# Kernel optimization log

Hardware: AMD Instinct MI355X
Metric: run time of the kernel (lower is better)

Reference implementation:

```python
import jax, jax.numpy as jnp
import numpy as np

B, L, D, H = 48, 512, 192, 6
DK = D // H
HID = 4 * D
EPS = 1e-5
SCALE = 1.0 / np.float32(np.sqrt(DK))


def _ln(x, g, b):
    mu = x.mean(-1, keepdims=True)
    v = ((x - mu) ** 2).mean(-1, keepdims=True)
    return (x - mu) * jax.lax.rsqrt(v + EPS) * g + b


def _mln(x, m, g, b):
    # masked layernorm: valid rows normalized, invalid rows pass through unchanged
    return jnp.where(m[..., None], _ln(x, g, b), x)


def _mha(q, k, v, mask, wq, bq, wk, bk, wv, bv, wo, bo):
    def proj(x, w, bb):
        return (x @ w + bb).reshape(B, L, H, DK).transpose(0, 2, 1, 3)  # [B,H,L,dk]
    Q, K, V = proj(q, wq, bq), proj(k, wk, bk), proj(v, wv, bv)
    s = jnp.einsum('bhqd,bhkd->bhqk', Q, K) * SCALE
    s = jnp.where(mask[:, None], -1e9, s)  # mask True = invalid pair
    p = jax.nn.softmax(s, axis=-1)
    o = jnp.einsum('bhqk,bhkd->bhqd', p, V).transpose(0, 2, 1, 3).reshape(B, L, D)
    return o @ wo + bo


def _forward(x_a, x_b, valid_a, valid_b,
             ln_a_g, ln_a_b, ln_b_g, ln_b_b, ln_oa_g, ln_oa_b, ln_ob_g, ln_ob_b,
             wq, bq, wk, bk, wv, bv, wo, bo,
             fln_g, fln_b, flno_g, flno_b, w1, b1, w2, b2):
    mB2A = ~(valid_a[:, :, None] & valid_b[:, None, :])  # [B,La,Lb]
    mA2B = ~(valid_b[:, :, None] & valid_a[:, None, :])
    a = _mln(x_a, valid_a, ln_a_g, ln_a_b)
    b = _mln(x_b, valid_b, ln_b_g, ln_b_b)
    oa = _mha(a, b, b, mB2A, wq, bq, wk, bk, wv, bv, wo, bo)
    oa = _mln(oa + x_a, valid_a, ln_oa_g, ln_oa_b)
    ob = _mha(b, a, a, mA2B, wq, bq, wk, bk, wv, bv, wo, bo)
    ob = _mln(ob + x_b, valid_b, ln_ob_g, ln_ob_b)

    def ffn(x, m):
        xn = _mln(x, m, fln_g, fln_b)
        y = jax.nn.gelu(xn @ w1 + b1, approximate=False) @ w2 + b2
        return _mln(x + y, m, flno_g, flno_b)

    return ffn(oa, valid_a), ffn(ob, valid_b)


def setup_inputs() -> dict:
    key = jax.random.key(0)
    ks = jax.random.split(key, 12)
    p = lambda k, s: jax.random.normal(k, s, dtype=jnp.float32) * 0.02
    ones = lambda s: jnp.ones(s, dtype=jnp.float32)
    zeros = lambda s: jnp.zeros(s, dtype=jnp.float32)
    return {
        'x_a': jax.random.normal(ks[0], (B, L, D), dtype=jnp.float32),
        'x_b': jax.random.normal(ks[1], (B, L, D), dtype=jnp.float32),
        'valid_a': jax.random.bernoulli(ks[2], 0.9, (B, L)),
        'valid_b': jax.random.bernoulli(ks[3], 0.9, (B, L)),
        'ln_a_g': ones((D,)), 'ln_a_b': zeros((D,)),
        'ln_b_g': ones((D,)), 'ln_b_b': zeros((D,)),
        'ln_oa_g': ones((D,)), 'ln_oa_b': zeros((D,)),
        'ln_ob_g': ones((D,)), 'ln_ob_b': zeros((D,)),
        'wq': p(ks[4], (D, D)), 'bq': zeros((D,)),
        'wk': p(ks[5], (D, D)), 'bk': zeros((D,)),
        'wv': p(ks[6], (D, D)), 'bv': zeros((D,)),
        'wo': p(ks[7], (D, D)), 'bo': zeros((D,)),
        'fln_g': ones((D,)), 'fln_b': zeros((D,)),
        'flno_g': ones((D,)), 'flno_b': zeros((D,)),
        'w1': p(ks[8], (D, HID)), 'b1': zeros((HID,)),
        'w2': p(ks[9], (HID, D)), 'b2': zeros((D,)),
    }


def reference(x_a, x_b, valid_a, valid_b,
              ln_a_g, ln_a_b, ln_b_g, ln_b_b, ln_oa_g, ln_oa_b, ln_ob_g, ln_ob_b,
              wq, bq, wk, bk, wv, bv, wo, bo,
              fln_g, fln_b, flno_g, flno_b, w1, b1, w2, b2):
    return _forward(x_a, x_b, valid_a, valid_b,
                    ln_a_g, ln_a_b, ln_b_g, ln_b_b, ln_oa_g, ln_oa_b, ln_ob_g, ln_ob_b,
                    wq, bq, wk, bk, wv, bv, wo, bo,
                    fln_g, fln_b, flno_g, flno_b, w1, b1, w2, b2)
```

## Files before the change

kernel.cpp:

```cpp
#include <hip/hip_runtime.h>
#include <math.h>

#define BB 48
#define LL 512
#define DD 192
#define HH 6
#define DKK 32
#define HID 768
#define ROWS (BB * LL)
#define BLD ((size_t)ROWS * DD)
#define SB2 0.25503531f
#define MASKED_X (-36.0f)

typedef unsigned short ushort_t;
typedef unsigned int uint_t;
typedef __bf16 bf16x8 __attribute__((ext_vector_type(8)));
typedef float f32x4 __attribute__((ext_vector_type(4)));

union U4BF8 { uint4 u; bf16x8 b; };
union BFU { __bf16 h; ushort_t u; };

__device__ __forceinline__ ushort_t f2bf(float f) {
  union { float f; uint_t u; } v; v.f = f;
  uint_t r = v.u + 0x7fffu + ((v.u >> 16) & 1u);
  return (ushort_t)(r >> 16);
}
__device__ __forceinline__ ushort_t cvt_bf(float f) {
  BFU c; c.h = (__bf16)f; return c.u;
}

__device__ __forceinline__ int swz_w(int n, int k, int N) {
  return ((k >> 5) * (N >> 4) + (n >> 4)) * 512 +
         ((((k & 31) >> 3) << 4) + (n & 15)) * 8 + (k & 7);
}

__global__ __launch_bounds__(256) void pack_kernel(
    const float* __restrict__ wq, const float* __restrict__ wk,
    const float* __restrict__ wv, const float* __restrict__ wo,
    const float* __restrict__ w1, const float* __restrict__ w2,
    const float* __restrict__ bq, const float* __restrict__ bk,
    const float* __restrict__ bv,
    ushort_t* __restrict__ Wqkv, ushort_t* __restrict__ Wo,
    ushort_t* __restrict__ W1, ushort_t* __restrict__ W2,
    float* __restrict__ bqkv) {
  int i = blockIdx.x * 256 + threadIdx.x;
  if (i < 110592) {
    int n2 = i / 192, k = i - n2 * 192;
    int part = n2 / 192, n = n2 - part * 192;
    const float* src = part == 0 ? wq : (part == 1 ? wk : wv);
    Wqkv[swz_w(n2, k, 576)] = f2bf(src[k * 192 + n]);
  } else if (i < 147456) {
    int j = i - 110592;
    int n = j / 192, k = j - n * 192;
    Wo[swz_w(n, k, 192)] = f2bf(wo[k * 192 + n]);
  } else if (i < 294912) {
    int j = i - 147456;
    int n = j / 192, k = j - n * 192;
    W1[j] = f2bf(w1[k * 768 + n]);
  } else if (i < 442368) {
    int j = i - 294912;
    int n = j / 768, k = j - n * 768;
    W2[j] = f2bf(w2[k * 192 + n]);
  } else if (i < 442944) {
    int j = i - 442368;
    bqkv[j] = j < 192 ? bq[j] : (j < 384 ? bk[j - 192] : bv[j - 384]);
  }
}

__global__ __launch_bounds__(256) void qkv_ln_kernel(
    const float* __restrict__ xa, const float* __restrict__ xb,
    const int* __restrict__ va, const int* __restrict__ vb,
    const float* __restrict__ g_a, const float* __restrict__ b_a,
    const float* __restrict__ g_b, const float* __restrict__ b_b,
    const ushort_t* __restrict__ Wsw, const float* __restrict__ bias,
    ushort_t* __restrict__ Cb) {
  constexpr int N = 576;
  constexpr int CSB = N + 8;
  __shared__ ushort_t smem[32 * CSB];
  ushort_t* As = smem;

  int tid = threadIdx.x;
  int w = tid >> 6, lane = tid & 63, l15 = lane & 15, kq = lane >> 4;
  int row0 = blockIdx.x * 32;
  int side = row0 >= ROWS;
  int rb = row0 - side * ROWS;

  {
    int row = tid >> 3, l8 = tid & 7;
    const float* xr = (side ? xb : xa) + (size_t)(rb + row) * DD + l8 * 24;
    float v[24];
    float s = 0.f;
#pragma unroll
    for (int j = 0; j < 6; ++j) {
      float4 q = *(const float4*)(xr + j * 4);
      v[j*4+0] = q.x; v[j*4+1] = q.y; v[j*4+2] = q.z; v[j*4+3] = q.w;
      s += q.x + q.y + q.z + q.w;
    }
    s += __shfl_xor(s, 1); s += __shfl_xor(s, 2); s += __shfl_xor(s, 4);
    float mu = s * (1.0f / 192.0f);
    float ss = 0.f;
#pragma unroll
    for (int j = 0; j < 24; ++j) { float d = v[j] - mu; ss += d * d; }
    ss += __shfl_xor(ss, 1); ss += __shfl_xor(ss, 2); ss += __shfl_xor(ss, 4);
    float inv = rsqrtf(ss * (1.0f / 192.0f) + 1e-5f);
    int vld = (side ? vb : va)[rb + row];
    const float* g = side ? g_b : g_a;
    const float* be = side ? b_b : b_a;
    ushort_t ob[24];
#pragma unroll
    for (int j = 0; j < 24; ++j) {
      int col = l8 * 24 + j;
      float r = vld ? (v[j] - mu) * inv * g[col] + be[col] : v[j];
      ob[j] = f2bf(r);
    }
#pragma unroll
    for (int j = 0; j < 3; ++j)
      *(uint4*)(&As[row * 200 + l8 * 24 + j * 8]) = *(const uint4*)(&ob[j * 8]);
  }
  __syncthreads();

  f32x4 acc[2][9];
#pragma unroll
  for (int qs = 0; qs < 2; ++qs)
#pragma unroll
    for (int nt = 0; nt < 9; ++nt) acc[qs][nt] = (f32x4){0.f, 0.f, 0.f, 0.f};

#pragma unroll 1
  for (int kk = 0; kk < 6; ++kk) {
    bf16x8 af[2];
#pragma unroll
    for (int qs = 0; qs < 2; ++qs)
      af[qs] = *(const bf16x8*)(&As[(qs * 16 + l15) * 200 + kk * 32 + kq * 8]);
    const ushort_t* wp =
        Wsw + ((size_t)(kk * (N >> 4) + w * 9) << 9) + lane * 8;
#pragma unroll
    for (int nt = 0; nt < 9; ++nt) {
      U4BF8 wf;
      wf.u = *(const uint4*)(wp + (nt << 9));
#pragma unroll
      for (int qs = 0; qs < 2; ++qs)
        acc[qs][nt] = __builtin_amdgcn_mfma_f32_16x16x32_bf16(
            af[qs], wf.b, acc[qs][nt], 0, 0, 0);
    }
  }
  __syncthreads();

  ushort_t* Cs = smem;
#pragma unroll
  for (int nt = 0; nt < 9; ++nt) {
    int col = (w * 9 + nt) * 16 + l15;
    float bb = bias[col];
#pragma unroll
    for (int qs = 0; qs < 2; ++qs)
#pragma unroll
      for (int r = 0; r < 4; ++r)
        Cs[(qs * 16 + kq * 4 + r) * CSB + col] = f2bf(acc[qs][nt][r] + bb);
  }
  __syncthreads();
  constexpr int UPR = (N * 2) / 16;
#pragma unroll
  for (int i = 0; i < (32 * UPR) / 256; ++i) {
    int idx = tid + i * 256;
    int r = idx / UPR, u = idx - r * UPR;
    *(uint4*)(Cb + (size_t)row0 * N + idx * 8) =
        *(const uint4*)(&Cs[r * CSB + u * 8]);
  }
}

__global__ __launch_bounds__(256) void oproj_ln_kernel(
    const ushort_t* __restrict__ A, const ushort_t* __restrict__ Wsw,
    const float* __restrict__ bias,
    const float* __restrict__ xa, const float* __restrict__ xb,
    const int* __restrict__ va, const int* __restrict__ vb,
    const float* __restrict__ g_oa, const float* __restrict__ b_oa,
    const float* __restrict__ g_ob, const float* __restrict__ b_ob,
    const float* __restrict__ g_f, const float* __restrict__ b_f,
    float* __restrict__ outf, ushort_t* __restrict__ outb) {
  __shared__ float smemf[32 * 196];
  ushort_t* As = (ushort_t*)smemf;

  int tid = threadIdx.x;
  int w = tid >> 6, lane = tid & 63, l15 = lane & 15, kq = lane >> 4;
  int row0 = blockIdx.x * 32;
  int side = row0 >= ROWS;
  int rb = row0 - side * ROWS;

  {
    const ushort_t* ap = A + (size_t)row0 * DD;
#pragma unroll
    for (int i = 0; i < 3; ++i) {
      int idx = tid + i * 256;
      int r = idx / 24, c = (idx - r * 24) * 8;
      *(uint4*)(&As[r * 200 + c]) = *(const uint4*)(ap + idx * 8);
    }
  }
  __syncthreads();

  f32x4 acc[2][3];
#pragma unroll
  for (int qs = 0; qs < 2; ++qs)
#pragma unroll
    for (int nt = 0; nt < 3; ++nt) acc[qs][nt] = (f32x4){0.f, 0.f, 0.f, 0.f};

#pragma unroll 1
  for (int kk = 0; kk < 6; ++kk) {
    bf16x8 af[2];
#pragma unroll
    for (int qs = 0; qs < 2; ++qs)
      af[qs] = *(const bf16x8*)(&As[(qs * 16 + l15) * 200 + kk * 32 + kq * 8]);
    const ushort_t* wp =
        Wsw + ((size_t)(kk * (192 >> 4) + w * 3) << 9) + lane * 8;
#pragma unroll
    for (int nt = 0; nt < 3; ++nt) {
      U4BF8 wf;
      wf.u = *(const uint4*)(wp + (nt << 9));
#pragma unroll
      for (int qs = 0; qs < 2; ++qs)
        acc[qs][nt] = __builtin_amdgcn_mfma_f32_16x16x32_bf16(
            af[qs], wf.b, acc[qs][nt], 0, 0, 0);
    }
  }
  __syncthreads();

  float* Cs = smemf;
#pragma unroll
  for (int nt = 0; nt < 3; ++nt) {
    int col = (w * 3 + nt) * 16 + l15;
    float bb = bias[col];
#pragma unroll
    for (int qs = 0; qs < 2; ++qs)
#pragma unroll
      for (int r = 0; r < 4; ++r)
        Cs[(qs * 16 + kq * 4 + r) * 196 + col] = acc[qs][nt][r] + bb;
  }
  __syncthreads();

  int row = tid >> 3, l8 = tid & 7;
  int grow = row0 + row;
  const float* xrow = (side ? xb : xa) + (size_t)(rb + row) * DD;
  const float* crow = &Cs[row * 196];
  float v[24];
  float s = 0.f;
#pragma unroll
  for (int j = 0; j < 6; ++j) {
    int col = j * 32 + l8 * 4;
    float4 q = *(const float4*)(xrow + col);
    v[j*4+0] = crow[col+0] + q.x; v[j*4+1] = crow[col+1] + q.y;
    v[j*4+2] = crow[col+2] + q.z; v[j*4+3] = crow[col+3] + q.w;
    s += v[j*4+0] + v[j*4+1] + v[j*4+2] + v[j*4+3];
  }
  s += __shfl_xor(s, 1); s += __shfl_xor(s, 2); s += __shfl_xor(s, 4);
  float mu = s * (1.0f / 192.0f);
  float ss = 0.f;
#pragma unroll
  for (int j = 0; j < 24; ++j) { float d = v[j] - mu; ss += d * d; }
  ss += __shfl_xor(ss, 1); ss += __shfl_xor(ss, 2); ss += __shfl_xor(ss, 4);
  float inv = rsqrtf(ss * (1.0f / 192.0f) + 1e-5f);
  int vld = (side ? vb : va)[rb + row];
  const float* g1 = side ? g_ob : g_oa;
  const float* b1 = side ? b_ob : b_oa;
  float y[24];
#pragma unroll
  for (int j = 0; j < 6; ++j) {
#pragma unroll
    for (int e = 0; e < 4; ++e) {
      int col = j * 32 + l8 * 4 + e;
      float vv = v[j * 4 + e];
      y[j * 4 + e] = vld ? (vv - mu) * inv * g1[col] + b1[col] : vv;
    }
  }
  float* orow = outf + (size_t)grow * DD;
#pragma unroll
  for (int j = 0; j < 6; ++j) {
    float4 q = {y[j*4+0], y[j*4+1], y[j*4+2], y[j*4+3]};
    *(float4*)(orow + j * 32 + l8 * 4) = q;
  }
  float s2 = 0.f;
#pragma unroll
  for (int j = 0; j < 24; ++j) s2 += y[j];
  s2 += __shfl_xor(s2, 1); s2 += __shfl_xor(s2, 2); s2 += __shfl_xor(s2, 4);
  float mu2 = s2 * (1.0f / 192.0f);
  float ss2 = 0.f;
#pragma unroll
  for (int j = 0; j < 24; ++j) { float e = y[j] - mu2; ss2 += e * e; }
  ss2 += __shfl_xor(ss2, 1); ss2 += __shfl_xor(ss2, 2); ss2 += __shfl_xor(ss2, 4);
  float inv2 = rsqrtf(ss2 * (1.0f / 192.0f) + 1e-5f);
  ushort_t* obrow = outb + (size_t)grow * DD;
#pragma unroll
  for (int j = 0; j < 6; ++j) {
    ushort_t zb[4];
#pragma unroll
    for (int e = 0; e < 4; ++e) {
      int col = j * 32 + l8 * 4 + e;
      float z = vld ? (y[j*4+e] - mu2) * inv2 * g_f[col] + b_f[col] : y[j*4+e];
      zb[e] = f2bf(z);
    }
    *(uint2*)(obrow + j * 32 + l8 * 4) = *(const uint2*)(&zb[0]);
  }
}

__global__ __launch_bounds__(256, 3) void ffn_fused_kernel(
    const ushort_t* __restrict__ A, const ushort_t* __restrict__ W1t,
    const float* __restrict__ bias1, const ushort_t* __restrict__ W2t,
    const float* __restrict__ bias2,
    const int* __restrict__ va, const int* __restrict__ vb,
    const float* __restrict__ g_f, const float* __restrict__ b_f,
    float* __restrict__ outf) {
  __shared__ float smemf[64 * 196];
  ushort_t* As = (ushort_t*)smemf;
  ushort_t* Hs = As + 64 * 200;

  int tid = threadIdx.x;
  int w = tid >> 6;
  int lane = tid & 63;
  int l15 = lane & 15;
  int kq = lane >> 4;
  int row0 = blockIdx.x * 64;
  int side = row0 >= ROWS;
  int rb0 = row0 - side * ROWS;

#pragma unroll
  for (int i = 0; i < 6; ++i) {
    int idx = tid + i * 256;
    int r = idx / 24, c = (idx % 24) * 8;
    *(uint4*)(&As[r * 200 + c]) = *(const uint4*)(A + (size_t)(row0 + r) * DD + c);
  }

  const ushort_t* w1p = W1t + (size_t)(w * 16 + l15) * DD + kq * 8;
  const ushort_t* w2p = W2t + (size_t)(w * 48 + l15) * HID + kq * 8;

  U4BF8 w1f[6], w1n[6], w2f[6];
#pragma unroll
  for (int kk = 0; kk < 6; ++kk)
    w1f[kk].u = *(const uint4*)(w1p + kk * 32);

  f32x4 Cacc[4][3];
#pragma unroll
  for (int qs = 0; qs < 4; ++qs)
#pragma unroll
    for (int nt = 0; nt < 3; ++nt) Cacc[qs][nt] = (f32x4){0.f, 0.f, 0.f, 0.f};

  __syncthreads();

  for (int hc = 0; hc < 12; ++hc) {
#pragma unroll
    for (int kk2 = 0; kk2 < 2; ++kk2)
#pragma unroll
      for (int nt = 0; nt < 3; ++nt)
        w2f[kk2 * 3 + nt].u =
            *(const uint4*)(w2p + (size_t)(nt * 16) * HID + hc * 64 + kk2 * 32);

    f32x4 Hacc[4];
#pragma unroll
    for (int qs = 0; qs < 4; ++qs) Hacc[qs] = (f32x4){0.f, 0.f, 0.f, 0.f};
#pragma unroll
    for (int kk = 0; kk < 6; ++kk) {
#pragma unroll
      for (int qs = 0; qs < 4; ++qs) {
        bf16x8 af = *(const bf16x8*)(&As[(qs * 16 + l15) * 200 + kk * 32 + kq * 8]);
        Hacc[qs] = __builtin_amdgcn_mfma_f32_16x16x32_bf16(
            af, w1f[kk].b, Hacc[qs], 0, 0, 0);
      }
    }

    if (hc < 11) {
#pragma unroll
      for (int kk = 0; kk < 6; ++kk)
        w1n[kk].u = *(const uint4*)(w1p + (size_t)(hc + 1) * 64 * DD + kk * 32);
    }

    {
      float bb = bias1[hc * 64 + w * 16 + l15];
      ushort_t* hb = &Hs[(hc & 1) * 4608];
#pragma unroll
      for (int qs = 0; qs < 4; ++qs)
#pragma unroll
        for (int r = 0; r < 4; ++r) {
          float x = Hacc[qs][r] + bb;
          x = 0.5f * x * (1.0f + erff(x * 0.70710678118654752f));
          hb[(qs * 16 + kq * 4 + r) * 72 + w * 16 + l15] = f2bf(x);
        }
    }
    __syncthreads();

#pragma unroll
    for (int kk2 = 0; kk2 < 2; ++kk2) {
      bf16x8 hf[4];
#pragma unroll
      for (int qs = 0; qs < 4; ++qs)
        hf[qs] = *(const bf16x8*)(&Hs[(hc & 1) * 4608 +
                                      (qs * 16 + l15) * 72 + kk2 * 32 + kq * 8]);
#pragma unroll
      for (int nt = 0; nt < 3; ++nt)
#pragma unroll
        for (int qs = 0; qs < 4; ++qs)
          Cacc[qs][nt] = __builtin_amdgcn_mfma_f32_16x16x32_bf16(
              hf[qs], w2f[kk2 * 3 + nt].b, Cacc[qs][nt], 0, 0, 0);
    }

#pragma unroll
    for (int kk = 0; kk < 6; ++kk) w1f[kk] = w1n[kk];
  }
  __syncthreads();

  float* Cs = smemf;
#pragma unroll
  for (int qs = 0; qs < 4; ++qs)
#pragma unroll
    for (int nt = 0; nt < 3; ++nt) {
      int col = w * 48 + nt * 16 + l15;
      float bb = bias2[col];
#pragma unroll
      for (int r = 0; r < 4; ++r)
        Cs[(qs * 16 + kq * 4 + r) * 196 + col] = Cacc[qs][nt][r] + bb;
    }
  __syncthreads();

  int row = tid >> 2, l4 = tid & 3;
  int grow = row0 + row;
  float* orow = outf + (size_t)grow * DD;
  const float* crow = &Cs[row * 196];
  float v[48];
  float s = 0.f;
#pragma unroll
  for (int j = 0; j < 12; ++j) {
    int col = j * 16 + l4 * 4;
    float4 q = *(const float4*)(orow + col);
    v[j*4+0] = crow[col+0] + q.x; v[j*4+1] = crow[col+1] + q.y;
    v[j*4+2] = crow[col+2] + q.z; v[j*4+3] = crow[col+3] + q.w;
    s += v[j*4+0] + v[j*4+1] + v[j*4+2] + v[j*4+3];
  }
  s += __shfl_xor(s, 1); s += __shfl_xor(s, 2);
  float mu = s * (1.0f / 192.0f);
  float ss = 0.f;
#pragma unroll
  for (int j = 0; j < 48; ++j) { float d = v[j] - mu; ss += d * d; }
  ss += __shfl_xor(ss, 1); ss += __shfl_xor(ss, 2);
  float inv = rsqrtf(ss * (1.0f / 192.0f) + 1e-5f);
  int vld = (side ? vb : va)[rb0 + row];
#pragma unroll
  for (int j = 0; j < 12; ++j) {
    int col = j * 16 + l4 * 4;
    float4 q;
#pragma unroll
    for (int e = 0; e < 4; ++e) {
      float vv = v[j * 4 + e];
      ((float*)&q)[e] = vld ? (vv - mu) * inv * g_f[col + e] + b_f[col + e] : vv;
    }
    *(float4*)(orow + col) = q;
  }
}

__global__ __launch_bounds__(256) void attn_mfma_kernel(
    const ushort_t* __restrict__ QKV,
    const int* __restrict__ valid_a, const int* __restrict__ valid_b,
    ushort_t* __restrict__ out) {
  int i = blockIdx.x;
  int gid = ((i >> 5) << 3) | (i & 7);
  int qt = (i >> 3) & 3;
  int side = gid >= BB * HH;
  int grem = side ? gid - BB * HH : gid;
  int h = grem % HH;
  int batch = grem / HH;
  int tid = threadIdx.x;
  int w = tid >> 6;
  int lane = tid & 63;
  int l15 = lane & 15;
  int kq = lane >> 4;

  const int* validq = side ? valid_b : valid_a;
  const int* validk = side ? valid_a : valid_b;
  size_t qrow0  = (size_t)side * ROWS + (size_t)batch * LL;
  size_t kvrow0 = (size_t)(1 - side) * ROWS + (size_t)batch * LL;

  __shared__ ushort_t VsT[2][32 * 72];
  __shared__ ushort_t Ps[4][32 * 72];

  int qbase = qt * 128 + w * 32;

  U4BF8 qfrag[2];
#pragma unroll
  for (int qs = 0; qs < 2; ++qs)
    qfrag[qs].u = *(const uint4*)(QKV + (qrow0 + qbase + qs * 16 + l15) * 576 +
                                  h * DKK + kq * 8);

  float sqf[2][4], mq[2][4];
#pragma unroll
  for (int qs = 0; qs < 2; ++qs)
#pragma unroll
    for (int r = 0; r < 4; ++r) {
      int vq = validq[batch * LL + qbase + qs * 16 + kq * 4 + r];
      sqf[qs][r] = vq ? SB2 : 0.0f;
      mq[qs][r]  = vq ? 0.0f : MASKED_X;
    }

  float lsum[2][4];
  f32x4 Oacc[2][2];
#pragma unroll
  for (int qs = 0; qs < 2; ++qs) {
#pragma unroll
    for (int r = 0; r < 4; ++r) lsum[qs][r] = 0.0f;
#pragma unroll
    for (int ds = 0; ds < 2; ++ds) Oacc[qs][ds] = (f32x4){0.f, 0.f, 0.f, 0.f};
  }

  uint4 vv = *(const uint4*)(QKV + (kvrow0 + lane) * 576 + 384 + h * DKK + w * 8);
  U4BF8 kf[4];
  int vki[4];
#pragma unroll
  for (int ks = 0; ks < 4; ++ks) {
    kf[ks].u = *(const uint4*)(QKV + (kvrow0 + ks * 16 + l15) * 576 +
                               192 + h * DKK + kq * 8);
    vki[ks] = validk[batch * LL + ks * 16 + l15];
  }

  for (int c = 0; c < LL; c += 64) {
    int buf = (c >> 6) & 1;
    {
      uint_t uu[4] = {vv.x, vv.y, vv.z, vv.w};
#pragma unroll
      for (int j = 0; j < 4; ++j) {
        VsT[buf][(w * 8 + 2 * j) * 72 + lane]     = (ushort_t)(uu[j] & 0xffffu);
        VsT[buf][(w * 8 + 2 * j + 1) * 72 + lane] = (ushort_t)(uu[j] >> 16);
      }
    }
    uint4 vvn;
    if (c + 64 < LL)
      vvn = *(const uint4*)(QKV + (kvrow0 + c + 64 + lane) * 576 +
                            384 + h * DKK + w * 8);
    __syncthreads();

    f32x4 S[2][4];
    __builtin_amdgcn_s_setprio(1);
#pragma unroll
    for (int ks = 0; ks < 4; ++ks)
#pragma unroll
      for (int qs = 0; qs < 2; ++qs) {
        f32x4 z = (f32x4){0.f, 0.f, 0.f, 0.f};
        S[qs][ks] = __builtin_amdgcn_mfma_f32_16x16x32_bf16(
            qfrag[qs].b, kf[ks].b, z, 0, 0, 0);
      }
    __builtin_amdgcn_s_setprio(0);

    float mkb[4];
#pragma unroll
    for (int ks = 0; ks < 4; ++ks) mkb[ks] = vki[ks] ? 0.0f : MASKED_X;

    U4BF8 kfn[4];
    int vkn[4];
    if (c + 64 < LL) {
#pragma unroll
      for (int ks = 0; ks < 4; ++ks) {
        kfn[ks].u = *(const uint4*)(QKV + (kvrow0 + c + 64 + ks * 16 + l15) * 576 +
                                    192 + h * DKK + kq * 8);
        vkn[ks] = validk[batch * LL + c + 64 + ks * 16 + l15];
      }
    }

#pragma unroll
    for (int qs = 0; qs < 2; ++qs)
#pragma unroll
      for (int ks = 0; ks < 4; ++ks)
#pragma unroll
        for (int r = 0; r < 4; ++r) {
          float xs = fmaf(S[qs][ks][r], sqf[qs][r], fminf(mq[qs][r], mkb[ks]));
          float p = __builtin_amdgcn_exp2f(xs);
          lsum[qs][r] += p;
          Ps[w][(qs * 16 + kq * 4 + r) * 72 + ks * 16 + l15] = cvt_bf(p);
        }

    __builtin_amdgcn_s_setprio(1);
#pragma unroll
    for (int kh = 0; kh < 2; ++kh) {
      bf16x8 pf[2], vf[2];
#pragma unroll
      for (int qs = 0; qs < 2; ++qs)
        pf[qs] = *(const bf16x8*)(&Ps[w][(qs * 16 + l15) * 72 + kh * 32 + kq * 8]);
#pragma unroll
      for (int ds = 0; ds < 2; ++ds)
        vf[ds] = *(const bf16x8*)(&VsT[buf][(ds * 16 + l15) * 72 + kh * 32 + kq * 8]);
#pragma unroll
      for (int qs = 0; qs < 2; ++qs)
#pragma unroll
        for (int ds = 0; ds < 2; ++ds)
          Oacc[qs][ds] = __builtin_amdgcn_mfma_f32_16x16x32_bf16(
              pf[qs], vf[ds], Oacc[qs][ds], 0, 0, 0);
    }
    __builtin_amdgcn_s_setprio(0);

    vv = vvn;
#pragma unroll
    for (int ks = 0; ks < 4; ++ks) { kf[ks] = kfn[ks]; vki[ks] = vkn[ks]; }
  }

#pragma unroll
  for (int qs = 0; qs < 2; ++qs)
#pragma unroll
    for (int r = 0; r < 4; ++r) {
      float sm = lsum[qs][r];
#pragma unroll
      for (int off = 1; off < 16; off <<= 1) sm += __shfl_xor(sm, off);
      lsum[qs][r] = sm;
    }

#pragma unroll
  for (int qs = 0; qs < 2; ++qs)
#pragma unroll
    for (int ds = 0; ds < 2; ++ds)
#pragma unroll
      for (int r = 0; r < 4; ++r) {
        int q = qbase + qs * 16 + kq * 4 + r;
        out[(qrow0 + q) * DD + h * DKK + ds * 16 + l15] =
            f2bf(Oacc[qs][ds][r] / lsum[qs][r]);
      }
}

extern "C" void kernel_launch(void* const* d_in, const int* in_sizes, int n_in,
                              void* d_out, int out_size, void* d_ws, size_t ws_size,
                              hipStream_t stream) {
  const float* x_a = (const float*)d_in[0];
  const float* x_b = (const float*)d_in[1];
  const int* valid_a = (const int*)d_in[2];
  const int* valid_b = (const int*)d_in[3];
  const float* ln_a_g = (const float*)d_in[4];
  const float* ln_a_b = (const float*)d_in[5];
  const float* ln_b_g = (const float*)d_in[6];
  const float* ln_b_b = (const float*)d_in[7];
  const float* ln_oa_g = (const float*)d_in[8];
  const float* ln_oa_b = (const float*)d_in[9];
  const float* ln_ob_g = (const float*)d_in[10];
  const float* ln_ob_b = (const float*)d_in[11];
  const float* wq = (const float*)d_in[12];
  const float* bq = (const float*)d_in[13];
  const float* wk = (const float*)d_in[14];
  const float* bk = (const float*)d_in[15];
  const float* wv = (const float*)d_in[16];
  const float* bv = (const float*)d_in[17];
  const float* wo = (const float*)d_in[18];
  const float* bo = (const float*)d_in[19];
  const float* fln_g = (const float*)d_in[20];
  const float* fln_b = (const float*)d_in[21];
  const float* flno_g = (const float*)d_in[22];
  const float* flno_b = (const float*)d_in[23];
  const float* w1 = (const float*)d_in[24];
  const float* b1 = (const float*)d_in[25];
  const float* w2 = (const float*)d_in[26];
  const float* b2 = (const float*)d_in[27];

  char* wsb = (char*)d_ws;
  ushort_t* Wqkv = (ushort_t*)wsb;
  ushort_t* Wo_t = Wqkv + 110592;
  ushort_t* W1_t = Wo_t + 36864;
  ushort_t* W2_t = W1_t + 147456;
  float*    bqkv = (float*)(W2_t + 147456);
  ushort_t* lnFull = (ushort_t*)(wsb + 887040);
  ushort_t* attO   = lnFull;
  ushort_t* QKV = (ushort_t*)(wsb + 19761408);

  float* out_a = (float*)d_out;

  dim3 b256(256);
  dim3 gGemm(2 * ROWS / 32);
  dim3 gAttn(BB * HH * 4 * 2);
  dim3 gFFN(2 * ROWS / 64);

  hipLaunchKernelGGL(pack_kernel, dim3(1731), b256, 0, stream,
                     wq, wk, wv, wo, w1, w2, bq, bk, bv,
                     Wqkv, Wo_t, W1_t, W2_t, bqkv);

  hipLaunchKernelGGL(qkv_ln_kernel, gGemm, b256, 0, stream,
                     x_a, x_b, valid_a, valid_b,
                     ln_a_g, ln_a_b, ln_b_g, ln_b_b,
                     Wqkv, bqkv, QKV);

  hipLaunchKernelGGL(attn_mfma_kernel, gAttn, b256, 0, stream,
                     QKV, valid_a, valid_b, attO);

  hipLaunchKernelGGL(oproj_ln_kernel, gGemm, b256, 0, stream,
                     attO, Wo_t, bo, x_a, x_b, valid_a, valid_b,
                     ln_oa_g, ln_oa_b, ln_ob_g, ln_ob_b, fln_g, fln_b,
                     out_a, lnFull);

  hipLaunchKernelGGL(ffn_fused_kernel, gFFN, b256, 0, stream,
                     lnFull, W1_t, b1, W2_t, b2, valid_a, valid_b,
                     flno_g, flno_b, out_a);
}
```

Baseline: 357.5 us.

## Shrink FFN tile to 32 rows with two waves covering wider columns

Restructures the fused FFN kernel to process 32 rows per block with 128 threads, where each wave computes 32 hidden columns and 96 output columns instead of 16 and 48. It removes the register double-buffered prefetch of W1 fragments and loads them inline per k-step, which lowers register pressure and doubles grid size for more parallelism. The trade-off is twice as many total weight fetches per row from L2, and W1 load latency is no longer hidden by prefetch.

```diff
diff --git a/kernel.cpp b/kernel.cpp
--- a/kernel.cpp
+++ b/kernel.cpp
@@ -299,116 +299,115 @@
   }
 }
 
-__global__ __launch_bounds__(256, 3) void ffn_fused_kernel(
+__global__ __launch_bounds__(128, 3) void ffn_fused_kernel(
     const ushort_t* __restrict__ A, const ushort_t* __restrict__ W1t,
     const float* __restrict__ bias1, const ushort_t* __restrict__ W2t,
     const float* __restrict__ bias2,
     const int* __restrict__ va, const int* __restrict__ vb,
     const float* __restrict__ g_f, const float* __restrict__ b_f,
     float* __restrict__ outf) {
-  __shared__ float smemf[64 * 196];
+  __shared__ float smemf[32 * 196];
   ushort_t* As = (ushort_t*)smemf;
-  ushort_t* Hs = As + 64 * 200;
+  ushort_t* Hs = As + 32 * 200;
 
   int tid = threadIdx.x;
   int w = tid >> 6;
   int lane = tid & 63;
   int l15 = lane & 15;
   int kq = lane >> 4;
-  int row0 = blockIdx.x * 64;
+  int row0 = blockIdx.x * 32;
   int side = row0 >= ROWS;
   int rb0 = row0 - side * ROWS;
 
 #pragma unroll
   for (int i = 0; i < 6; ++i) {
-    int idx = tid + i * 256;
+    int idx = tid + i * 128;
     int r = idx / 24, c = (idx % 24) * 8;
     *(uint4*)(&As[r * 200 + c]) = *(const uint4*)(A + (size_t)(row0 + r) * DD + c);
   }
 
-  const ushort_t* w1p = W1t + (size_t)(w * 16 + l15) * DD + kq * 8;
-  const ushort_t* w2p = W2t + (size_t)(w * 48 + l15) * HID + kq * 8;
-
-  U4BF8 w1f[6], w1n[6], w2f[6];
-#pragma unroll
-  for (int kk = 0; kk < 6; ++kk)
-    w1f[kk].u = *(const uint4*)(w1p + kk * 32);
-
-  f32x4 Cacc[4][3];
-#pragma unroll
-  for (int qs = 0; qs < 4; ++qs)
-#pragma unroll
-    for (int nt = 0; nt < 3; ++nt) Cacc[qs][nt] = (f32x4){0.f, 0.f, 0.f, 0.f};
+  const ushort_t* w1p = W1t + (size_t)(w * 32 + l15) * DD + kq * 8;
+  const ushort_t* w2p = W2t + (size_t)(w * 96 + l15) * HID + kq * 8;
+
+  f32x4 Cacc[2][6];
+#pragma unroll
+  for (int qs = 0; qs < 2; ++qs)
+#pragma unroll
+    for (int nt = 0; nt < 6; ++nt) Cacc[qs][nt] = (f32x4){0.f, 0.f, 0.f, 0.f};
 
   __syncthreads();
 
   for (int hc = 0; hc < 12; ++hc) {
+    U4BF8 w2f[12];
 #pragma unroll
     for (int kk2 = 0; kk2 < 2; ++kk2)
 #pragma unroll
-      for (int nt = 0; nt < 3; ++nt)
-        w2f[kk2 * 3 + nt].u =
+      for (int nt = 0; nt < 6; ++nt)
+        w2f[kk2 * 6 + nt].u =
             *(const uint4*)(w2p + (size_t)(nt * 16) * HID + hc * 64 + kk2 * 32);
 
-    f32x4 Hacc[4];
-#pragma unroll
-    for (int qs = 0; qs < 4; ++qs) Hacc[qs] = (f32x4){0.f, 0.f, 0.f, 0.f};
+    f32x4 Hacc[2][2];
+#pragma unroll
+    for (int qs = 0; qs < 2; ++qs)
+#pragma unroll
+      for (int nt = 0; nt < 2; ++nt) Hacc[qs][nt] = (f32x4){0.f, 0.f, 0.f, 0.f};
 #pragma unroll
     for (int kk = 0; kk < 6; ++kk) {
-#pragma unroll
-      for (int qs = 0; qs < 4; ++qs) {
-        bf16x8 af = *(const bf16x8*)(&As[(qs * 16 + l15) * 200 + kk * 32 + kq * 8]);
-        Hacc[qs] = __builtin_amdgcn_mfma_f32_16x16x32_bf16(
-            af, w1f[kk].b, Hacc[qs], 0, 0, 0);
+      bf16x8 af[2];
+#pragma unroll
+      for (int qs = 0; qs < 2; ++qs)
+        af[qs] = *(const bf16x8*)(&As[(qs * 16 + l15) * 200 + kk * 32 + kq * 8]);
+#pragma unroll
+      for (int nt = 0; nt < 2; ++nt) {
+        U4BF8 wf;
+        wf.u = *(const uint4*)(w1p + (size_t)(hc * 64 + nt * 16) * DD + kk * 32);
+#pragma unroll
+        for (int qs = 0; qs < 2; ++qs)
+          Hacc[qs][nt] = __builtin_amdgcn_mfma_f32_16x16x32_bf16(
+              af[qs], wf.b, Hacc[qs][nt], 0, 0, 0);
       }
     }
 
-    if (hc < 11) {
-#pragma unroll
-      for (int kk = 0; kk < 6; ++kk)
-        w1n[kk].u = *(const uint4*)(w1p + (size_t)(hc + 1) * 64 * DD + kk * 32);
-    }
-
     {
-      float bb = bias1[hc * 64 + w * 16 + l15];
-      ushort_t* hb = &Hs[(hc & 1) * 4608];
-#pragma unroll
-      for (int qs = 0; qs < 4; ++qs)
-#pragma unroll
-        for (int r = 0; r < 4; ++r) {
-          float x = Hacc[qs][r] + bb;
-          x = 0.5f * x * (1.0f + erff(x * 0.70710678118654752f));
-          hb[(qs * 16 + kq * 4 + r) * 72 + w * 16 + l15] = f2bf(x);
-        }
+      ushort_t* hb = &Hs[(hc & 1) * 2304];
+#pragma unroll
+      for (int nt = 0; nt < 2; ++nt) {
+        float bb = bias1[hc * 64 + w * 32 + nt * 16 + l15];
+#pragma unroll
+        for (int qs = 0; qs < 2; ++qs)
+#pragma unroll
+          for (int r = 0; r < 4; ++r) {
+            float x = Hacc[qs][nt][r] + bb;
+            x = 0.5f * x * (1.0f + erff(x * 0.70710678118654752f));
+            hb[(qs * 16 + kq * 4 + r) * 72 + w * 32 + nt * 16 + l15] = f2bf(x);
+          }
+      }
     }
     __syncthreads();
 
 #pragma unroll
     for (int kk2 = 0; kk2 < 2; ++kk2) {
-      bf16x8 hf[4];
-#pragma unroll
-      for (int qs = 0; qs < 4; ++qs)
-        hf[qs] = *(const bf16x8*)(&Hs[(hc & 1) * 4608 +
+      bf16x8 hf[2];
+#pragma unroll
+      for (int qs = 0; qs < 2; ++qs)
+        hf[qs] = *(const bf16x8*)(&Hs[(hc & 1) * 2304 +
                                       (qs * 16 + l15) * 72 + kk2 * 32 + kq * 8]);
 #pragma unroll
-      for (int nt = 0; nt < 3; ++nt)
-#pragma unroll
-        for (int qs = 0; qs < 4; ++qs)
+      for (int nt = 0; nt < 6; ++nt)
+#pragma unroll
+        for (int qs = 0; qs < 2; ++qs)
           Cacc[qs][nt] = __builtin_amdgcn_mfma_f32_16x16x32_bf16(
-              hf[qs], w2f[kk2 * 3 + nt].b, Cacc[qs][nt], 0, 0, 0);
-    }
-
-#pragma unroll
-    for (int kk = 0; kk < 6; ++kk) w1f[kk] = w1n[kk];
+              hf[qs], w2f[kk2 * 6 + nt].b, Cacc[qs][nt], 0, 0, 0);
+    }
   }
   __syncthreads();
 
   float* Cs = smemf;
 #pragma unroll
-  for (int qs = 0; qs < 4; ++qs)
-#pragma unroll
-    for (int nt = 0; nt < 3; ++nt) {
-      int col = w * 48 + nt * 16 + l15;
+  for (int qs = 0; qs < 2; ++qs)
+#pragma unroll
+    for (int nt = 0; nt < 6; ++nt) {
+      int col = w * 96 + nt * 16 + l15;
       float bb = bias2[col];
 #pragma unroll
       for (int r = 0; r < 4; ++r)
@@ -659,10 +658,10 @@
 
   float* out_a = (float*)d_out;
 
-  dim3 b256(256);
+  dim3 b128(128), b256(256);
   dim3 gGemm(2 * ROWS / 32);
   dim3 gAttn(BB * HH * 4 * 2);
-  dim3 gFFN(2 * ROWS / 64);
+  dim3 gFFN(2 * ROWS / 32);
 
   hipLaunchKernelGGL(pack_kernel, dim3(1731), b256, 0, stream,
                      wq, wk, wv, wo, w1, w2, bq, bk, bv,
@@ -681,7 +680,7 @@
                      ln_oa_g, ln_oa_b, ln_ob_g, ln_ob_b, fln_g, fln_b,
                      out_a, lnFull);
 
-  hipLaunchKernelGGL(ffn_fused_kernel, gFFN, b256, 0, stream,
+  hipLaunchKernelGGL(ffn_fused_kernel, gFFN, b128, 0, stream,
                      lnFull, W1_t, b1, W2_t, b2, valid_a, valid_b,
                      flno_g, flno_b, out_a);
 }
```

Result: slower. 404.6 us (+13.2%).

## Fuse output projection and layernorms into FFN kernel, keep residual in registers

Applied to the files above, without the earlier changes.

Merges the O-projection and double-layernorm kernel into the fused FFN kernel, so each 64-row block computes the Wo GEMM, both layernorms, and then the FFN without writing the fp32 residual and the bf16 normalized activations to global memory and reading them back. The residual is held in registers (y[48]) across the FFN, and the normalized bf16 rows are written directly into shared memory as the FFN input. This removes one launch and a round trip of intermediates through global memory. In exchange it raises register pressure under a launch bound of 3 blocks per SM, which may cause spills or lower occupancy, and the O-projection now runs with 64-row tiles instead of 32.

```diff
diff --git a/kernel.cpp b/kernel.cpp
--- a/kernel.cpp
+++ b/kernel.cpp
@@ -167,154 +167,25 @@
   }
 }
 
-__global__ __launch_bounds__(256) void oproj_ln_kernel(
-    const ushort_t* __restrict__ A, const ushort_t* __restrict__ Wsw,
-    const float* __restrict__ bias,
+__global__ __launch_bounds__(256, 3) void oproj_ffn_kernel(
+    const ushort_t* __restrict__ A, const ushort_t* __restrict__ Wosw,
+    const float* __restrict__ bo,
     const float* __restrict__ xa, const float* __restrict__ xb,
     const int* __restrict__ va, const int* __restrict__ vb,
     const float* __restrict__ g_oa, const float* __restrict__ b_oa,
     const float* __restrict__ g_ob, const float* __restrict__ b_ob,
     const float* __restrict__ g_f, const float* __restrict__ b_f,
-    float* __restrict__ outf, ushort_t* __restrict__ outb) {
-  __shared__ float smemf[32 * 196];
-  ushort_t* As = (ushort_t*)smemf;
-
-  int tid = threadIdx.x;
-  int w = tid >> 6, lane = tid & 63, l15 = lane & 15, kq = lane >> 4;
-  int row0 = blockIdx.x * 32;
-  int side = row0 >= ROWS;
-  int rb = row0 - side * ROWS;
-
-  {
-    const ushort_t* ap = A + (size_t)row0 * DD;
-#pragma unroll
-    for (int i = 0; i < 3; ++i) {
-      int idx = tid + i * 256;
-      int r = idx / 24, c = (idx - r * 24) * 8;
-      *(uint4*)(&As[r * 200 + c]) = *(const uint4*)(ap + idx * 8);
-    }
-  }
-  __syncthreads();
-
-  f32x4 acc[2][3];
-#pragma unroll
-  for (int qs = 0; qs < 2; ++qs)
-#pragma unroll
-    for (int nt = 0; nt < 3; ++nt) acc[qs][nt] = (f32x4){0.f, 0.f, 0.f, 0.f};
-
-#pragma unroll 1
-  for (int kk = 0; kk < 6; ++kk) {
-    bf16x8 af[2];
-#pragma unroll
-    for (int qs = 0; qs < 2; ++qs)
-      af[qs] = *(const bf16x8*)(&As[(qs * 16 + l15) * 200 + kk * 32 + kq * 8]);
-    const ushort_t* wp =
-        Wsw + ((size_t)(kk * (192 >> 4) + w * 3) << 9) + lane * 8;
-#pragma unroll
-    for (int nt = 0; nt < 3; ++nt) {
-      U4BF8 wf;
-      wf.u = *(const uint4*)(wp + (nt << 9));
-#pragma unroll
-      for (int qs = 0; qs < 2; ++qs)
-        acc[qs][nt] = __builtin_amdgcn_mfma_f32_16x16x32_bf16(
-            af[qs], wf.b, acc[qs][nt], 0, 0, 0);
-    }
-  }
-  __syncthreads();
-
-  float* Cs = smemf;
-#pragma unroll
-  for (int nt = 0; nt < 3; ++nt) {
-    int col = (w * 3 + nt) * 16 + l15;
-    float bb = bias[col];
-#pragma unroll
-    for (int qs = 0; qs < 2; ++qs)
-#pragma unroll
-      for (int r = 0; r < 4; ++r)
-        Cs[(qs * 16 + kq * 4 + r) * 196 + col] = acc[qs][nt][r] + bb;
-  }
-  __syncthreads();
-
-  int row = tid >> 3, l8 = tid & 7;
-  int grow = row0 + row;
-  const float* xrow = (side ? xb : xa) + (size_t)(rb + row) * DD;
-  const float* crow = &Cs[row * 196];
-  float v[24];
-  float s = 0.f;
-#pragma unroll
-  for (int j = 0; j < 6; ++j) {
-    int col = j * 32 + l8 * 4;
-    float4 q = *(const float4*)(xrow + col);
-    v[j*4+0] = crow[col+0] + q.x; v[j*4+1] = crow[col+1] + q.y;
-    v[j*4+2] = crow[col+2] + q.z; v[j*4+3] = crow[col+3] + q.w;
-    s += v[j*4+0] + v[j*4+1] + v[j*4+2] + v[j*4+3];
-  }
-  s += __shfl_xor(s, 1); s += __shfl_xor(s, 2); s += __shfl_xor(s, 4);
-  float mu = s * (1.0f / 192.0f);
-  float ss = 0.f;
-#pragma unroll
-  for (int j = 0; j < 24; ++j) { float d = v[j] - mu; ss += d * d; }
-  ss += __shfl_xor(ss, 1); ss += __shfl_xor(ss, 2); ss += __shfl_xor(ss, 4);
-  float inv = rsqrtf(ss * (1.0f / 192.0f) + 1e-5f);
-  int vld = (side ? vb : va)[rb + row];
-  const float* g1 = side ? g_ob : g_oa;
-  const float* b1 = side ? b_ob : b_oa;
-  float y[24];
-#pragma unroll
-  for (int j = 0; j < 6; ++j) {
-#pragma unroll
-    for (int e = 0; e < 4; ++e) {
-      int col = j * 32 + l8 * 4 + e;
-      float vv = v[j * 4 + e];
-      y[j * 4 + e] = vld ? (vv - mu) * inv * g1[col] + b1[col] : vv;
-    }
-  }
-  float* orow = outf + (size_t)grow * DD;
-#pragma unroll
-  for (int j = 0; j < 6; ++j) {
-    float4 q = {y[j*4+0], y[j*4+1], y[j*4+2], y[j*4+3]};
-    *(float4*)(orow + j * 32 + l8 * 4) = q;
-  }
-  float s2 = 0.f;
-#pragma unroll
-  for (int j = 0; j < 24; ++j) s2 += y[j];
-  s2 += __shfl_xor(s2, 1); s2 += __shfl_xor(s2, 2); s2 += __shfl_xor(s2, 4);
-  float mu2 = s2 * (1.0f / 192.0f);
-  float ss2 = 0.f;
-#pragma unroll
-  for (int j = 0; j < 24; ++j) { float e = y[j] - mu2; ss2 += e * e; }
-  ss2 += __shfl_xor(ss2, 1); ss2 += __shfl_xor(ss2, 2); ss2 += __shfl_xor(ss2, 4);
-  float inv2 = rsqrtf(ss2 * (1.0f / 192.0f) + 1e-5f);
-  ushort_t* obrow = outb + (size_t)grow * DD;
-#pragma unroll
-  for (int j = 0; j < 6; ++j) {
-    ushort_t zb[4];
-#pragma unroll
-    for (int e = 0; e < 4; ++e) {
-      int col = j * 32 + l8 * 4 + e;
-      float z = vld ? (y[j*4+e] - mu2) * inv2 * g_f[col] + b_f[col] : y[j*4+e];
-      zb[e] = f2bf(z);
-    }
-    *(uint2*)(obrow + j * 32 + l8 * 4) = *(const uint2*)(&zb[0]);
-  }
-}
-
-__global__ __launch_bounds__(256, 3) void ffn_fused_kernel(
-    const ushort_t* __restrict__ A, const ushort_t* __restrict__ W1t,
-    const float* __restrict__ bias1, const ushort_t* __restrict__ W2t,
-    const float* __restrict__ bias2,
-    const int* __restrict__ va, const int* __restrict__ vb,
-    const float* __restrict__ g_f, const float* __restrict__ b_f,
+    const ushort_t* __restrict__ W1t, const float* __restrict__ bias1,
+    const ushort_t* __restrict__ W2t, const float* __restrict__ bias2,
+    const float* __restrict__ g_fo, const float* __restrict__ b_fo,
     float* __restrict__ outf) {
   __shared__ float smemf[64 * 196];
   ushort_t* As = (ushort_t*)smemf;
   ushort_t* Hs = As + 64 * 200;
+  float* Cs = smemf;
 
   int tid = threadIdx.x;
-  int w = tid >> 6;
-  int lane = tid & 63;
-  int l15 = lane & 15;
-  int kq = lane >> 4;
+  int w = tid >> 6, lane = tid & 63, l15 = lane & 15, kq = lane >> 4;
   int row0 = blockIdx.x * 64;
   int side = row0 >= ROWS;
   int rb0 = row0 - side * ROWS;
@@ -325,6 +196,99 @@
     int r = idx / 24, c = (idx % 24) * 8;
     *(uint4*)(&As[r * 200 + c]) = *(const uint4*)(A + (size_t)(row0 + r) * DD + c);
   }
+  __syncthreads();
+
+  f32x4 Cacc[4][3];
+#pragma unroll
+  for (int qs = 0; qs < 4; ++qs)
+#pragma unroll
+    for (int nt = 0; nt < 3; ++nt) Cacc[qs][nt] = (f32x4){0.f, 0.f, 0.f, 0.f};
+
+#pragma unroll 1
+  for (int kk = 0; kk < 6; ++kk) {
+    bf16x8 af[4];
+#pragma unroll
+    for (int qs = 0; qs < 4; ++qs)
+      af[qs] = *(const bf16x8*)(&As[(qs * 16 + l15) * 200 + kk * 32 + kq * 8]);
+    const ushort_t* wp = Wosw + ((size_t)(kk * 12 + w * 3) << 9) + lane * 8;
+#pragma unroll
+    for (int nt = 0; nt < 3; ++nt) {
+      U4BF8 wf;
+      wf.u = *(const uint4*)(wp + (nt << 9));
+#pragma unroll
+      for (int qs = 0; qs < 4; ++qs)
+        Cacc[qs][nt] = __builtin_amdgcn_mfma_f32_16x16x32_bf16(
+            af[qs], wf.b, Cacc[qs][nt], 0, 0, 0);
+    }
+  }
+  __syncthreads();
+
+#pragma unroll
+  for (int qs = 0; qs < 4; ++qs)
+#pragma unroll
+    for (int nt = 0; nt < 3; ++nt) {
+      int col = w * 48 + nt * 16 + l15;
+      float bb = bo[col];
+#pragma unroll
+      for (int r = 0; r < 4; ++r)
+        Cs[(qs * 16 + kq * 4 + r) * 196 + col] = Cacc[qs][nt][r] + bb;
+    }
+  __syncthreads();
+
+  int row = tid >> 2, l4 = tid & 3;
+  int vld = (side ? vb : va)[rb0 + row];
+  const float* xrow = (side ? xb : xa) + (size_t)(rb0 + row) * DD;
+  const float* crow = &Cs[row * 196];
+  const float* g1 = side ? g_ob : g_oa;
+  const float* b1 = side ? b_ob : b_oa;
+  float y[48];
+  float s = 0.f;
+#pragma unroll
+  for (int j = 0; j < 12; ++j) {
+    int col = j * 16 + l4 * 4;
+    float4 q = *(const float4*)(xrow + col);
+    y[j*4+0] = crow[col+0] + q.x; y[j*4+1] = crow[col+1] + q.y;
+    y[j*4+2] = crow[col+2] + q.z; y[j*4+3] = crow[col+3] + q.w;
+    s += y[j*4+0] + y[j*4+1] + y[j*4+2] + y[j*4+3];
+  }
+  s += __shfl_xor(s, 1); s += __shfl_xor(s, 2);
+  float mu = s * (1.0f / 192.0f);
+  float ss = 0.f;
+#pragma unroll
+  for (int j = 0; j < 48; ++j) { float d = y[j] - mu; ss += d * d; }
+  ss += __shfl_xor(ss, 1); ss += __shfl_xor(ss, 2);
+  float inv = rsqrtf(ss * (1.0f / 192.0f) + 1e-5f);
+#pragma unroll
+  for (int j = 0; j < 12; ++j)
+#pragma unroll
+    for (int e = 0; e < 4; ++e) {
+      int col = j * 16 + l4 * 4 + e;
+      float vv = y[j * 4 + e];
+      y[j * 4 + e] = vld ? (vv - mu) * inv * g1[col] + b1[col] : vv;
+    }
+  float s2 = 0.f;
+#pragma unroll
+  for (int j = 0; j < 48; ++j) s2 += y[j];
+  s2 += __shfl_xor(s2, 1); s2 += __shfl_xor(s2, 2);
+  float mu2 = s2 * (1.0f / 192.0f);
+  float ss2 = 0.f;
+#pragma unroll
+  for (int j = 0; j < 48; ++j) { float e = y[j] - mu2; ss2 += e * e; }
+  ss2 += __shfl_xor(ss2, 1); ss2 += __shfl_xor(ss2, 2);
+  float inv2 = rsqrtf(ss2 * (1.0f / 192.0f) + 1e-5f);
+  ushort_t z[48];
+#pragma unroll
+  for (int j = 0; j < 12; ++j)
+#pragma unroll
+    for (int e = 0; e < 4; ++e) {
+      int col = j * 16 + l4 * 4 + e;
+      float zz = vld ? (y[j*4+e] - mu2) * inv2 * g_f[col] + b_f[col] : y[j*4+e];
+      z[j * 4 + e] = f2bf(zz);
+    }
+  __syncthreads();
+#pragma unroll
+  for (int j = 0; j < 12; ++j)
+    *(uint2*)(&As[row * 200 + j * 16 + l4 * 4]) = *(const uint2*)(&z[j * 4]);
 
   const ushort_t* w1p = W1t + (size_t)(w * 16 + l15) * DD + kq * 8;
   const ushort_t* w2p = W2t + (size_t)(w * 48 + l15) * HID + kq * 8;
@@ -334,11 +298,11 @@
   for (int kk = 0; kk < 6; ++kk)
     w1f[kk].u = *(const uint4*)(w1p + kk * 32);
 
-  f32x4 Cacc[4][3];
+  f32x4 Facc[4][3];
 #pragma unroll
   for (int qs = 0; qs < 4; ++qs)
 #pragma unroll
-    for (int nt = 0; nt < 3; ++nt) Cacc[qs][nt] = (f32x4){0.f, 0.f, 0.f, 0.f};
+    for (int nt = 0; nt < 3; ++nt) Facc[qs][nt] = (f32x4){0.f, 0.f, 0.f, 0.f};
 
   __syncthreads();
 
@@ -394,8 +358,8 @@
       for (int nt = 0; nt < 3; ++nt)
 #pragma unroll
         for (int qs = 0; qs < 4; ++qs)
-          Cacc[qs][nt] = __builtin_amdgcn_mfma_f32_16x16x32_bf16(
-              hf[qs], w2f[kk2 * 3 + nt].b, Cacc[qs][nt], 0, 0, 0);
+          Facc[qs][nt] = __builtin_amdgcn_mfma_f32_16x16x32_bf16(
+              hf[qs], w2f[kk2 * 3 + nt].b, Facc[qs][nt], 0, 0, 0);
     }
 
 #pragma unroll
@@ -403,7 +367,6 @@
   }
   __syncthreads();
 
-  float* Cs = smemf;
 #pragma unroll
   for (int qs = 0; qs < 4; ++qs)
 #pragma unroll
@@ -412,40 +375,37 @@
       float bb = bias2[col];
 #pragma unroll
       for (int r = 0; r < 4; ++r)
-        Cs[(qs * 16 + kq * 4 + r) * 196 + col] = Cacc[qs][nt][r] + bb;
-    }
-  __syncthreads();
-
-  int row = tid >> 2, l4 = tid & 3;
-  int grow = row0 + row;
-  float* orow = outf + (size_t)grow * DD;
-  const float* crow = &Cs[row * 196];
-  float v[48];
-  float s = 0.f;
+        Cs[(qs * 16 + kq * 4 + r) * 196 + col] = Facc[qs][nt][r] + bb;
+    }
+  __syncthreads();
+
+  float* orow = outf + (size_t)(row0 + row) * DD;
+  float s3 = 0.f;
 #pragma unroll
   for (int j = 0; j < 12; ++j) {
     int col = j * 16 + l4 * 4;
-    float4 q = *(const float4*)(orow + col);
-    v[j*4+0] = crow[col+0] + q.x; v[j*4+1] = crow[col+1] + q.y;
-    v[j*4+2] = crow[col+2] + q.z; v[j*4+3] = crow[col+3] + q.w;
-    s += v[j*4+0] + v[j*4+1] + v[j*4+2] + v[j*4+3];
-  }
-  s += __shfl_xor(s, 1); s += __shfl_xor(s, 2);
-  float mu = s * (1.0f / 192.0f);
-  float ss = 0.f;
-#pragma unroll
-  for (int j = 0; j < 48; ++j) { float d = v[j] - mu; ss += d * d; }
-  ss += __shfl_xor(ss, 1); ss += __shfl_xor(ss, 2);
-  float inv = rsqrtf(ss * (1.0f / 192.0f) + 1e-5f);
-  int vld = (side ? vb : va)[rb0 + row];
+#pragma unroll
+    for (int e = 0; e < 4; ++e) {
+      y[j * 4 + e] += crow[col + e];
+      s3 += y[j * 4 + e];
+    }
+  }
+  s3 += __shfl_xor(s3, 1); s3 += __shfl_xor(s3, 2);
+  float mu3 = s3 * (1.0f / 192.0f);
+  float ss3 = 0.f;
+#pragma unroll
+  for (int j = 0; j < 48; ++j) { float d = y[j] - mu3; ss3 += d * d; }
+  ss3 += __shfl_xor(ss3, 1); ss3 += __shfl_xor(ss3, 2);
+  float inv3 = rsqrtf(ss3 * (1.0f / 192.0f) + 1e-5f);
 #pragma unroll
   for (int j = 0; j < 12; ++j) {
     int col = j * 16 + l4 * 4;
     float4 q;
 #pragma unroll
     for (int e = 0; e < 4; ++e) {
-      float vv = v[j * 4 + e];
-      ((float*)&q)[e] = vld ? (vv - mu) * inv * g_f[col + e] + b_f[col + e] : vv;
+      float vv = y[j * 4 + e];
+      ((float*)&q)[e] =
+          vld ? (vv - mu3) * inv3 * g_fo[col + e] + b_fo[col + e] : vv;
     }
     *(float4*)(orow + col) = q;
   }
@@ -653,8 +613,7 @@
   ushort_t* W1_t = Wo_t + 36864;
   ushort_t* W2_t = W1_t + 147456;
   float*    bqkv = (float*)(W2_t + 147456);
-  ushort_t* lnFull = (ushort_t*)(wsb + 887040);
-  ushort_t* attO   = lnFull;
+  ushort_t* attO = (ushort_t*)(wsb + 887040);
   ushort_t* QKV = (ushort_t*)(wsb + 19761408);
 
   float* out_a = (float*)d_out;
@@ -662,7 +621,7 @@
   dim3 b256(256);
   dim3 gGemm(2 * ROWS / 32);
   dim3 gAttn(BB * HH * 4 * 2);
-  dim3 gFFN(2 * ROWS / 64);
+  dim3 gOF(2 * ROWS / 64);
 
   hipLaunchKernelGGL(pack_kernel, dim3(1731), b256, 0, stream,
                      wq, wk, wv, wo, w1, w2, bq, bk, bv,
@@ -676,12 +635,9 @@
   hipLaunchKernelGGL(attn_mfma_kernel, gAttn, b256, 0, stream,
                      QKV, valid_a, valid_b, attO);
 
-  hipLaunchKernelGGL(oproj_ln_kernel, gGemm, b256, 0, stream,
+  hipLaunchKernelGGL(oproj_ffn_kernel, gOF, b256, 0, stream,
                      attO, Wo_t, bo, x_a, x_b, valid_a, valid_b,
                      ln_oa_g, ln_oa_b, ln_ob_g, ln_ob_b, fln_g, fln_b,
-                     out_a, lnFull);
-
-  hipLaunchKernelGGL(ffn_fused_kernel, gFFN, b256, 0, stream,
-                     lnFull, W1_t, b1, W2_t, b2, valid_a, valid_b,
-                     flno_g, flno_b, out_a);
-}
+                     W1_t, b1, W2_t, b2, flno_g, flno_b,
+                     out_a);
+}
```

After: 367.9 us. 1.03x slower.
